# Optimization experiments

Measured on AMD Instinct MI355X. Metric: run time of the kernel, lower is better.

Reference implementation:

```python
import jax, jax.numpy as jnp
import numpy as np

B, C, HH, WW = 4, 128, 64, 64
NH = 2                      # n_heads
D = C // NH                 # head dim
N = HH * WW                 # tokens


def setup_inputs() -> dict:
    key = jax.random.key(0)
    ks = jax.random.split(key, 8)
    s = 1.0 / np.sqrt(C)
    return {
        "x": jax.random.normal(ks[0], (B, C, HH, WW), dtype=jnp.float32),
        "wq": jax.random.normal(ks[1], (C, C), dtype=jnp.float32) * s,
        "bq": jnp.zeros((C,), dtype=jnp.float32),
        "wk": jax.random.normal(ks[2], (C, C), dtype=jnp.float32) * s,
        "bk": jnp.zeros((C,), dtype=jnp.float32),
        "wv": jax.random.normal(ks[3], (C, C), dtype=jnp.float32) * s,
        "bv": jnp.zeros((C,), dtype=jnp.float32),
        "pe": jax.random.normal(ks[4], (N, D, NH), dtype=jnp.float32),
    }


def reference(x, wq, bq, wk, bk, wv, bv, pe):
    b, c, h, w = x.shape
    nh = pe.shape[2]
    d = c // nh
    n = h * w
    xf = x.reshape(b, c, n)                       # flatten spatial -> tokens
    # 1x1 convs == per-pixel channel matmuls
    q = jnp.einsum('oc,bcn->bon', wq, xf) + bq[None, :, None]
    k = jnp.einsum('oc,bcn->bon', wk, xf) + bk[None, :, None]
    v = jnp.einsum('oc,bcn->bon', wv, xf) + bv[None, :, None]
    q = q.reshape(b, nh, d, n)
    k = k.reshape(b, nh, d, n)
    v = v.reshape(b, nh, d, n)
    # learned positional encoding added to q: pe [n, d, nh] -> [nh, d, n]
    q = q + jnp.transpose(pe, (2, 1, 0))[None]
    scale = jnp.asarray(c, x.dtype) ** -0.25
    scores = jnp.einsum('bhdn,bhdm->bhnm', q, k) * scale   # [b,nh,n,n]
    attn = jax.nn.softmax(scores, axis=-1)
    # dropout is identity in eval mode
    o = jnp.einsum('bhnm,bhdm->bhdn', attn, v)             # [b,nh,d,n]
    attn_out = jnp.transpose(o.reshape(b, nh, d, h, w), (0, 2, 1, 3, 4))
    out = attn_out.reshape(b, c, h, w)
    return (out, attn_out)
```

## Files before the change

kernel.cpp:

```cpp
#include <hip/hip_runtime.h>
#include <hip/hip_bf16.h>

typedef unsigned short ushort_t;
typedef unsigned int   uint_t;
typedef unsigned short ushortx8 __attribute__((ext_vector_type(8)));
typedef unsigned short ushortx4 __attribute__((ext_vector_type(4)));
typedef unsigned int   uintx4   __attribute__((ext_vector_type(4)));
typedef __bf16        bf16x8   __attribute__((ext_vector_type(8)));
typedef float         f32x4    __attribute__((ext_vector_type(4)));
typedef float         f32x16   __attribute__((ext_vector_type(16)));

#define SCALE_QL (0.29730177875068026f * 1.4426950408889634f)
#define OUT_HALF 2097152
#define NSPLIT   4
#define KT_SPLIT 16
#define MFIX     32.0f

static __device__ __forceinline__ float fexp2(float x) {
    float r; asm("v_exp_f32 %0, %1" : "=v"(r) : "v"(x)); return r;
}
static __device__ __forceinline__ unsigned cvtpk_bf16(float lo, float hi) {
    unsigned r;
    asm("v_cvt_pk_bf16_f32 %0, %1, %2" : "=v"(r) : "v"(lo), "v"(hi));
    return r;
}
static __device__ __forceinline__ void pswap(unsigned& a, unsigned& b) {
    asm("v_permlane32_swap_b32 %0, %1" : "+v"(a), "+v"(b));
}
static __device__ __forceinline__ ushort_t bf16u(float f) {
    __hip_bfloat16 h = __float2bfloat16(f);
    return __builtin_bit_cast(ushort_t, h);
}
static __device__ __forceinline__ float bflo(unsigned u) {
    return __builtin_bit_cast(float, u << 16);
}
static __device__ __forceinline__ float bfhi(unsigned u) {
    return __builtin_bit_cast(float, u & 0xffff0000u);
}
static __device__ __forceinline__ void glds16(const void* g, void* l) {
    __builtin_amdgcn_global_load_lds(
        (const __attribute__((address_space(1))) unsigned int*)g,
        (__attribute__((address_space(3))) unsigned int*)l, 16, 0, 0);
}

__global__ __launch_bounds__(256) void prep_kernel(
    const float* __restrict__ pe,
    const float* __restrict__ wq, const float* __restrict__ wk,
    const float* __restrict__ wv,
    float* __restrict__ pet, ushort_t* __restrict__ wb)
{
    const int bid = blockIdx.x, t = threadIdx.x;
    if (bid < 1024) {
        int idx = bid * 256 + t;
        float2 p2 = *(const float2*)(pe + (size_t)idx * 2);
        pet[idx]                     = p2.x;
        pet[(size_t)4096 * 64 + idx] = p2.y;
        return;
    }
    const int b2 = bid - 1024;
    const int p  = b2 >> 3;
    const float* w = (p == 0) ? wq : (p == 1) ? wk : wv;
    const int cid = (b2 & 7) * 256 + t;
    const int o = cid >> 4, chunk = cid & 15;
    float4 f0 = *(const float4*)(w + o * 128 + chunk * 8);
    float4 f1 = *(const float4*)(w + o * 128 + chunk * 8 + 4);
    ushortx8 u;
    u[0] = bf16u(f0.x); u[1] = bf16u(f0.y); u[2] = bf16u(f0.z); u[3] = bf16u(f0.w);
    u[4] = bf16u(f1.x); u[5] = bf16u(f1.y); u[6] = bf16u(f1.z); u[7] = bf16u(f1.w);
    *(ushortx8*)(wb + p * 16384 + o * 128 + ((chunk ^ (o & 15)) << 3)) = u;
}

__global__ __launch_bounds__(256) void xt_kernel(const float* __restrict__ x,
                                                 ushort_t* __restrict__ xtb)
{
    const int nt = blockIdx.x, b = blockIdx.y;
    __shared__ __align__(16) ushort_t xs[128][68];
    const int t = threadIdx.x;
    const int cg = t >> 4, n0 = (t & 15) * 4;
#pragma unroll
    for (int i = 0; i < 8; ++i) {
        int c = i * 16 + cg;
        float4 f = *(const float4*)(x + ((size_t)(b * 128 + c)) * 4096 + nt * 64 + n0);
        ushortx4 u;
        u[0] = bf16u(f.x); u[1] = bf16u(f.y); u[2] = bf16u(f.z); u[3] = bf16u(f.w);
        *(ushortx4*)(&xs[c][n0]) = u;
    }
    __syncthreads();
    const int n = t >> 2;
    ushort_t* dst = xtb + ((size_t)b * 4096 + nt * 64 + n) * 128;
#pragma unroll
    for (int j = 0; j < 4; ++j) {
        int chunk = (t & 3) * 4 + j;
        ushortx8 u;
#pragma unroll
        for (int e = 0; e < 8; ++e) u[e] = xs[chunk * 8 + e][n];
        *(ushortx8*)(dst + ((chunk ^ (n & 15)) << 3)) = u;
    }
}

__global__ __launch_bounds__(256, 2) void proj_kernel(
    const ushort_t* __restrict__ xtb, const ushort_t* __restrict__ wb,
    const float* __restrict__ bq, const float* __restrict__ bk,
    const float* __restrict__ bv, const float* __restrict__ pet,
    ushort_t* __restrict__ qw, ushort_t* __restrict__ kw,
    ushort_t* __restrict__ vw)
{
    const int ntl = blockIdx.x;
    const int b = blockIdx.y, p = blockIdx.z;
    __shared__ __align__(16) ushort_t xt[16384];
    __shared__ __align__(16) ushort_t wt[16384];
    const int t = threadIdx.x, lane = t & 63;
    const int wv_ = __builtin_amdgcn_readfirstlane(t >> 6);
    const int l16 = lane & 15, lhi = lane >> 4;

    const ushort_t* xsrc = xtb + ((size_t)b * 4096 + ntl * 128) * 128;
    const ushort_t* wsrc = wb + p * 16384;
#pragma unroll
    for (int j = 0; j < 8; ++j) {
        int row = wv_ * 32 + j * 4;
        glds16(xsrc + row * 128 + lane * 8, xt + row * 128);
        glds16(wsrc + row * 128 + lane * 8, wt + row * 128);
    }

    const float* bias = (p == 0) ? bq : (p == 1) ? bk : bv;
    f32x4 bias4[2];
    bias4[0] = *(const f32x4*)(bias + wv_ * 32 + lhi * 4);
    bias4[1] = *(const f32x4*)(bias + wv_ * 32 + 16 + lhi * 4);
    f32x4 acc[2][8];
#pragma unroll
    for (int mf = 0; mf < 2; ++mf)
#pragma unroll
        for (int nf = 0; nf < 8; ++nf) acc[mf][nf] = bias4[mf];

    __syncthreads();

    const char* xbp = (const char*)xt;
    const char* wbp = (const char*)wt;
#pragma unroll
    for (int ks = 0; ks < 4; ++ks) {
        bf16x8 af[2];
#pragma unroll
        for (int mf = 0; mf < 2; ++mf) {
            int row = wv_ * 32 + mf * 16 + l16;
            af[mf] = __builtin_bit_cast(bf16x8, *(const ushortx8*)(
                wbp + row * 256 + ((((ks * 4 + lhi) ^ l16) & 15) << 4)));
        }
#pragma unroll
        for (int nf = 0; nf < 8; ++nf) {
            int row = nf * 16 + l16;
            bf16x8 bfr = __builtin_bit_cast(bf16x8, *(const ushortx8*)(
                xbp + row * 256 + ((((ks * 4 + lhi) ^ l16) & 15) << 4)));
            acc[0][nf] = __builtin_amdgcn_mfma_f32_16x16x32_bf16(af[0], bfr, acc[0][nf], 0, 0, 0);
            acc[1][nf] = __builtin_amdgcn_mfma_f32_16x16x32_bf16(af[1], bfr, acc[1][nf], 0, 0, 0);
        }
    }

    const int nbase = ntl * 128;
    if (p == 2) {
#pragma unroll
        for (int mf = 0; mf < 2; ++mf) {
            int o = wv_ * 32 + mf * 16 + lhi * 4;
            int h = o >> 6, d = o & 63;
            ushort_t* vb = vw + (((size_t)(b * 2 + h) * 64 + d)) * 4096 + nbase + l16;
#pragma unroll
            for (int nf = 0; nf < 8; ++nf)
#pragma unroll
                for (int r = 0; r < 4; ++r)
                    vb[(size_t)r * 4096 + nf * 16] = bf16u(acc[mf][nf][r]);
        }
    } else if (p == 0) {
#pragma unroll
        for (int mf = 0; mf < 2; ++mf) {
            int o = wv_ * 32 + mf * 16 + lhi * 4;
            int h = o >> 6, d = o & 63;
#pragma unroll
            for (int nf = 0; nf < 8; ++nf) {
                int n = nbase + nf * 16 + l16;
                f32x4 pe4 = *(const f32x4*)(pet + ((size_t)h * 4096 + n) * 64 + d);
                f32x4 q4 = (acc[mf][nf] + pe4) * SCALE_QL;
                ushortx4 s;
                s[0] = bf16u(q4[0]); s[1] = bf16u(q4[1]);
                s[2] = bf16u(q4[2]); s[3] = bf16u(q4[3]);
                *(ushortx4*)(qw + ((size_t)(b * 2 + h) * 4096 + n) * 64 + d) = s;
            }
        }
    } else {
#pragma unroll
        for (int mf = 0; mf < 2; ++mf) {
            int o = wv_ * 32 + mf * 16 + lhi * 4;
            int h = o >> 6, d = o & 63;
#pragma unroll
            for (int nf = 0; nf < 8; ++nf) {
                int n = nbase + nf * 16 + l16;
                f32x4 k4 = acc[mf][nf];
                ushortx4 s;
                s[0] = bf16u(k4[0]); s[1] = bf16u(k4[1]);
                s[2] = bf16u(k4[2]); s[3] = bf16u(k4[3]);
                *(ushortx4*)(kw + ((size_t)(b * 2 + h) * 4096 + n) * 64 + d) = s;
            }
        }
    }
}

__global__ __launch_bounds__(512, 4) void attn_kernel(
    const ushort_t* __restrict__ qw, const ushort_t* __restrict__ kw,
    const ushort_t* __restrict__ vw, uint_t* __restrict__ opart,
    float* __restrict__ lspart)
{
    const int qt = blockIdx.x, bh = blockIdx.y, sp = blockIdx.z;
    const int t = threadIdx.x, lane = t & 63;
    const int wv = t >> 6;
    const int l31 = lane & 31, hi = lane >> 5;

    __shared__ __align__(16) ushort_t Kt[2 * 64 * 64];
    __shared__ __align__(16) ushort_t Vt[2 * 64 * 64];

    const int qb = qt * 256 + wv * 32;
    bf16x8 qf[4];
#pragma unroll
    for (int ks = 0; ks < 4; ++ks)
        qf[ks] = __builtin_bit_cast(bf16x8, *(const ushortx8*)(
            qw + ((size_t)bh * 4096 + qb + l31) * 64 + ks * 16 + hi * 8));

    const ushort_t* kgb = kw + ((size_t)bh * 4096) * 64;
    const ushort_t* vgb = vw + ((size_t)bh * 64) * 4096;

    const int srow = lane >> 3, c7 = lane & 7;
    const int rb = wv * 8;
    const int swz = (c7 ^ srow) << 3;
    const size_t koff = (size_t)(rb + srow) * 64 + swz;
    const size_t voff = (size_t)(rb + srow) * 4096 + swz;

    const f32x16 z16 = {0,0,0,0,0,0,0,0,0,0,0,0,0,0,0,0};
    f32x16 oa0 = z16, oa1 = z16;
    float ls0 = 0.f;

    const int kt0 = sp * KT_SPLIT;

#define STAGE(buf, ktb)                                                       \
    {                                                                         \
        glds16(kgb + (size_t)(ktb) * 4096 + koff,                             \
               Kt + (buf) * 4096 + (size_t)rb * 64);                          \
        glds16(vgb + (size_t)(ktb) * 64 + voff,                               \
               Vt + (buf) * 4096 + (size_t)rb * 64);                          \
    }

    STAGE(0, kt0)
    __syncthreads();

    const int sw7 = l31 & 7;
    int cur = 0;
    for (int it = 0; it < KT_SPLIT; ++it) {
        const int itn = (it + 1 < KT_SPLIT) ? it + 1 : it;
        STAGE(cur ^ 1, kt0 + itn)

        const char* kc = (const char*)(Kt + cur * 4096);
        const char* vc = (const char*)(Vt + cur * 4096);

#pragma unroll
        for (int c = 0; c < 2; ++c) {
            const int kbase = (c * 32 + l31) * 128;
            bf16x8 kf[4];
#pragma unroll
            for (int ks = 0; ks < 4; ++ks)
                kf[ks] = __builtin_bit_cast(bf16x8, *(const ushortx8*)(
                    kc + kbase + (((ks * 2 + hi) ^ sw7) << 4)));

            f32x16 s0 = z16;
            __builtin_amdgcn_s_setprio(1);
#pragma unroll
            for (int ks = 0; ks < 4; ++ks)
                s0 = __builtin_amdgcn_mfma_f32_32x32x16_bf16(kf[ks], qf[ks], s0, 0, 0, 0);
            __builtin_amdgcn_s_setprio(0);

            float p[16];
#pragma unroll
            for (int r = 0; r < 16; ++r) p[r] = fexp2(s0[r] - MFIX);
            float q0 = (p[0] + p[1]) + (p[2] + p[3]);
            float q1 = (p[4] + p[5]) + (p[6] + p[7]);
            float q2 = (p[8] + p[9]) + (p[10] + p[11]);
            float q3 = (p[12] + p[13]) + (p[14] + p[15]);
            float psum = (q0 + q1) + (q2 + q3);
            psum += __shfl_xor(psum, 32, 64);
            ls0 += psum;
            unsigned c0 = cvtpk_bf16(p[0], p[1]);
            unsigned c1 = cvtpk_bf16(p[2], p[3]);
            unsigned c2 = cvtpk_bf16(p[4], p[5]);
            unsigned c3 = cvtpk_bf16(p[6], p[7]);
            unsigned c4 = cvtpk_bf16(p[8], p[9]);
            unsigned c5 = cvtpk_bf16(p[10], p[11]);
            unsigned c6 = cvtpk_bf16(p[12], p[13]);
            unsigned c7x = cvtpk_bf16(p[14], p[15]);
            pswap(c0, c2); pswap(c1, c3); pswap(c4, c6); pswap(c5, c7x);
            bf16x8 pfa, pfb;
            { uintx4 u; u[0] = c0; u[1] = c1; u[2] = c2; u[3] = c3;
              pfa = __builtin_bit_cast(bf16x8, u); }
            { uintx4 u; u[0] = c4; u[1] = c5; u[2] = c6; u[3] = c7x;
              pfb = __builtin_bit_cast(bf16x8, u); }

            __builtin_amdgcn_s_setprio(1);
            {
                const int vb0 = l31 * 128;
                bf16x8 vf0 = __builtin_bit_cast(bf16x8, *(const ushortx8*)(
                    vc + vb0 + ((((c * 2 + 0) * 2 + hi) ^ sw7) << 4)));
                bf16x8 vf1 = __builtin_bit_cast(bf16x8, *(const ushortx8*)(
                    vc + vb0 + ((((c * 2 + 1) * 2 + hi) ^ sw7) << 4)));
                oa0 = __builtin_amdgcn_mfma_f32_32x32x16_bf16(vf0, pfa, oa0, 0, 0, 0);
                oa0 = __builtin_amdgcn_mfma_f32_32x32x16_bf16(vf1, pfb, oa0, 0, 0, 0);
            }
            {
                const int vb1 = (32 + l31) * 128;
                bf16x8 vf0 = __builtin_bit_cast(bf16x8, *(const ushortx8*)(
                    vc + vb1 + ((((c * 2 + 0) * 2 + hi) ^ sw7) << 4)));
                bf16x8 vf1 = __builtin_bit_cast(bf16x8, *(const ushortx8*)(
                    vc + vb1 + ((((c * 2 + 1) * 2 + hi) ^ sw7) << 4)));
                oa1 = __builtin_amdgcn_mfma_f32_32x32x16_bf16(vf0, pfa, oa1, 0, 0, 0);
                oa1 = __builtin_amdgcn_mfma_f32_32x32x16_bf16(vf1, pfb, oa1, 0, 0, 0);
            }
            __builtin_amdgcn_s_setprio(0);
        }

        __syncthreads();
        cur ^= 1;
    }

    const int pidx = (qt * 8 + bh) * NSPLIT + sp;
#define STORE_OA(OA, DT)                                                      \
    {                                                                         \
        uintx4 u0, u1;                                                        \
        u0[0] = cvtpk_bf16(OA[0], OA[1]);  u0[1] = cvtpk_bf16(OA[2], OA[3]);  \
        u0[2] = cvtpk_bf16(OA[4], OA[5]);  u0[3] = cvtpk_bf16(OA[6], OA[7]);  \
        u1[0] = cvtpk_bf16(OA[8], OA[9]);  u1[1] = cvtpk_bf16(OA[10], OA[11]);\
        u1[2] = cvtpk_bf16(OA[12], OA[13]);u1[3] = cvtpk_bf16(OA[14], OA[15]);\
        uint_t* dst = opart +                                                 \
            (((size_t)pidx * 8 + wv) * 2 + (DT)) * 512 + lane * 8;            \
        *(uintx4*)dst = u0; *(uintx4*)(dst + 4) = u1;                         \
    }
    STORE_OA(oa0, 0) STORE_OA(oa1, 1)

    if (hi == 0)
        lspart[(pidx * 8 + wv) * 32 + l31] = ls0;
}

__global__ __launch_bounds__(512) void combine_kernel(
    const uint_t* __restrict__ opart, const float* __restrict__ lspart,
    float* __restrict__ out)
{
    const int qt = blockIdx.x, bh = blockIdx.y;
    const int b = bh >> 1, h = bh & 1;
    const int t = threadIdx.x, lane = t & 63, wa = t >> 6;
    const int l31 = lane & 31, hi = lane >> 5;
    const int pbase = (qt * 8 + bh) * NSPLIT;
    const int dtbl[8] = {0, 2, 8, 10, 16, 18, 24, 26};

    float den = 0.f;
#pragma unroll
    for (int sp = 0; sp < NSPLIT; ++sp)
        den += lspart[((pbase + sp) * 8 + wa) * 32 + l31];
    float inv = 1.f / den;

    const int q = qt * 256 + wa * 32 + l31;
#pragma unroll
    for (int dt = 0; dt < 2; ++dt) {
        float acc[16];
#pragma unroll
        for (int i = 0; i < 16; ++i) acc[i] = 0.f;
#pragma unroll
        for (int sp = 0; sp < NSPLIT; ++sp) {
            const uint_t* src = opart +
                (((size_t)(pbase + sp) * 8 + wa) * 2 + dt) * 512 + lane * 8;
            uintx4 a = *(const uintx4*)src;
            uintx4 b2 = *(const uintx4*)(src + 4);
#pragma unroll
            for (int j = 0; j < 4; ++j) {
                acc[2 * j]     += bflo(a[j]);
                acc[2 * j + 1] += bfhi(a[j]);
                acc[8 + 2 * j] += bflo(b2[j]);
                acc[9 + 2 * j] += bfhi(b2[j]);
            }
        }
#pragma unroll
        for (int j = 0; j < 8; ++j) {
            int d = dt * 32 + 4 * hi + dtbl[j];
            float v0 = acc[2 * j] * inv;
            float v1 = acc[2 * j + 1] * inv;
            size_t o0 = ((size_t)(b * 128 + d * 2 + h)) * 4096 + q;
            out[o0] = v0;
            out[o0 + OUT_HALF] = v0;
            size_t o1 = o0 + 2 * 4096;
            out[o1] = v1;
            out[o1 + OUT_HALF] = v1;
        }
    }
}

extern "C" void kernel_launch(void* const* d_in, const int* in_sizes, int n_in,
                              void* d_out, int out_size, void* d_ws, size_t ws_size,
                              hipStream_t stream) {
    const float* x  = (const float*)d_in[0];
    const float* wq = (const float*)d_in[1];
    const float* bq = (const float*)d_in[2];
    const float* wk = (const float*)d_in[3];
    const float* bk = (const float*)d_in[4];
    const float* wv = (const float*)d_in[5];
    const float* bv = (const float*)d_in[6];
    const float* pe = (const float*)d_in[7];
    float* out = (float*)d_out;

    char* ws = (char*)d_ws;
    float*    pet   = (float*)ws;
    ushort_t* qw    = (ushort_t*)(ws + (size_t)2  * 1024 * 1024);
    ushort_t* kw    = (ushort_t*)(ws + (size_t)6  * 1024 * 1024);
    ushort_t* vw    = (ushort_t*)(ws + (size_t)10 * 1024 * 1024);
    uint_t*   opart = (uint_t*)(ws + (size_t)14 * 1024 * 1024);
    ushort_t* xtb   = (ushort_t*)(ws + (size_t)14 * 1024 * 1024);
    float*    lsprt = (float*)(ws + (size_t)31 * 1024 * 1024);
    ushort_t* wb    = (ushort_t*)(ws + (size_t)31 * 1024 * 1024);

    hipLaunchKernelGGL(prep_kernel, dim3(1048), dim3(256), 0, stream,
                       pe, wq, wk, wv, pet, wb);
    hipLaunchKernelGGL(xt_kernel, dim3(64, 4), dim3(256), 0, stream, x, xtb);
    hipLaunchKernelGGL(proj_kernel, dim3(32, 4, 3), dim3(256), 0, stream,
                       xtb, wb, bq, bk, bv, pet, qw, kw, vw);
    hipLaunchKernelGGL(attn_kernel, dim3(16, 8, NSPLIT), dim3(512), 0, stream,
                       qw, kw, vw, opart, lsprt);
    hipLaunchKernelGGL(combine_kernel, dim3(16, 8), dim3(512), 0, stream,
                       opart, lsprt, out);
}
```

Baseline: 76.10 us.

## Fuse x transpose into projection kernel and loop over Q/K/V per block

Drops the separate xt_kernel. The projection kernel now loads fp32 x directly, converts it to bf16 and transposes it in shared memory, then loops over the three weight matrices (Q, K, V) reusing the same x tile. This removes one kernel launch and the global round trip through the xtb buffer, at the cost of a smaller token tile per block (64 instead of 128) and serialized weight loads inside each block. Separately, the attention kernel's cross-half row-sum shuffle is moved out of the inner loop to a single shuffle at the end.

```diff
diff --git a/kernel.cpp b/kernel.cpp
--- a/kernel.cpp
+++ b/kernel.cpp
@@ -70,133 +70,134 @@
     *(ushortx8*)(wb + p * 16384 + o * 128 + ((chunk ^ (o & 15)) << 3)) = u;
 }
 
-__global__ __launch_bounds__(256) void xt_kernel(const float* __restrict__ x,
-                                                 ushort_t* __restrict__ xtb)
-{
-    const int nt = blockIdx.x, b = blockIdx.y;
-    __shared__ __align__(16) ushort_t xs[128][68];
-    const int t = threadIdx.x;
-    const int cg = t >> 4, n0 = (t & 15) * 4;
-#pragma unroll
-    for (int i = 0; i < 8; ++i) {
-        int c = i * 16 + cg;
-        float4 f = *(const float4*)(x + ((size_t)(b * 128 + c)) * 4096 + nt * 64 + n0);
-        ushortx4 u;
-        u[0] = bf16u(f.x); u[1] = bf16u(f.y); u[2] = bf16u(f.z); u[3] = bf16u(f.w);
-        *(ushortx4*)(&xs[c][n0]) = u;
-    }
-    __syncthreads();
-    const int n = t >> 2;
-    ushort_t* dst = xtb + ((size_t)b * 4096 + nt * 64 + n) * 128;
-#pragma unroll
-    for (int j = 0; j < 4; ++j) {
-        int chunk = (t & 3) * 4 + j;
-        ushortx8 u;
-#pragma unroll
-        for (int e = 0; e < 8; ++e) u[e] = xs[chunk * 8 + e][n];
-        *(ushortx8*)(dst + ((chunk ^ (n & 15)) << 3)) = u;
-    }
-}
-
 __global__ __launch_bounds__(256, 2) void proj_kernel(
-    const ushort_t* __restrict__ xtb, const ushort_t* __restrict__ wb,
+    const float* __restrict__ x, const ushort_t* __restrict__ wb,
     const float* __restrict__ bq, const float* __restrict__ bk,
     const float* __restrict__ bv, const float* __restrict__ pet,
     ushort_t* __restrict__ qw, ushort_t* __restrict__ kw,
     ushort_t* __restrict__ vw)
 {
     const int ntl = blockIdx.x;
-    const int b = blockIdx.y, p = blockIdx.z;
-    __shared__ __align__(16) ushort_t xt[16384];
-    __shared__ __align__(16) ushort_t wt[16384];
+    const int b = blockIdx.y;
+    __shared__ __align__(16) ushort_t xt[64 * 128];
+    __shared__ __align__(16) union {
+        ushort_t xs[128][68];
+        ushort_t wt[16384];
+    } smu;
     const int t = threadIdx.x, lane = t & 63;
     const int wv_ = __builtin_amdgcn_readfirstlane(t >> 6);
     const int l16 = lane & 15, lhi = lane >> 4;
 
-    const ushort_t* xsrc = xtb + ((size_t)b * 4096 + ntl * 128) * 128;
-    const ushort_t* wsrc = wb + p * 16384;
-#pragma unroll
-    for (int j = 0; j < 8; ++j) {
-        int row = wv_ * 32 + j * 4;
-        glds16(xsrc + row * 128 + lane * 8, xt + row * 128);
-        glds16(wsrc + row * 128 + lane * 8, wt + row * 128);
-    }
-
-    const float* bias = (p == 0) ? bq : (p == 1) ? bk : bv;
-    f32x4 bias4[2];
-    bias4[0] = *(const f32x4*)(bias + wv_ * 32 + lhi * 4);
-    bias4[1] = *(const f32x4*)(bias + wv_ * 32 + 16 + lhi * 4);
-    f32x4 acc[2][8];
-#pragma unroll
-    for (int mf = 0; mf < 2; ++mf)
-#pragma unroll
-        for (int nf = 0; nf < 8; ++nf) acc[mf][nf] = bias4[mf];
-
+    {
+        const int cg = t >> 4, n0 = (t & 15) * 4;
+#pragma unroll
+        for (int i = 0; i < 8; ++i) {
+            int c = i * 16 + cg;
+            float4 f = *(const float4*)(x + ((size_t)(b * 128 + c)) * 4096 + ntl * 64 + n0);
+            ushortx4 u;
+            u[0] = bf16u(f.x); u[1] = bf16u(f.y); u[2] = bf16u(f.z); u[3] = bf16u(f.w);
+            *(ushortx4*)(&smu.xs[c][n0]) = u;
+        }
+    }
     __syncthreads();
-
+    {
+        const int n = t >> 2;
+#pragma unroll
+        for (int j = 0; j < 4; ++j) {
+            int chunk = (t & 3) * 4 + j;
+            ushortx8 u;
+#pragma unroll
+            for (int e = 0; e < 8; ++e) u[e] = smu.xs[chunk * 8 + e][n];
+            *(ushortx8*)(xt + n * 128 + ((chunk ^ (n & 15)) << 3)) = u;
+        }
+    }
+
+    const int nbase = ntl * 64;
     const char* xbp = (const char*)xt;
-    const char* wbp = (const char*)wt;
-#pragma unroll
-    for (int ks = 0; ks < 4; ++ks) {
-        bf16x8 af[2];
-#pragma unroll
-        for (int mf = 0; mf < 2; ++mf) {
-            int row = wv_ * 32 + mf * 16 + l16;
-            af[mf] = __builtin_bit_cast(bf16x8, *(const ushortx8*)(
-                wbp + row * 256 + ((((ks * 4 + lhi) ^ l16) & 15) << 4)));
-        }
-#pragma unroll
-        for (int nf = 0; nf < 8; ++nf) {
-            int row = nf * 16 + l16;
-            bf16x8 bfr = __builtin_bit_cast(bf16x8, *(const ushortx8*)(
-                xbp + row * 256 + ((((ks * 4 + lhi) ^ l16) & 15) << 4)));
-            acc[0][nf] = __builtin_amdgcn_mfma_f32_16x16x32_bf16(af[0], bfr, acc[0][nf], 0, 0, 0);
-            acc[1][nf] = __builtin_amdgcn_mfma_f32_16x16x32_bf16(af[1], bfr, acc[1][nf], 0, 0, 0);
-        }
-    }
-
-    const int nbase = ntl * 128;
-    if (p == 2) {
-#pragma unroll
-        for (int mf = 0; mf < 2; ++mf) {
-            int o = wv_ * 32 + mf * 16 + lhi * 4;
-            int h = o >> 6, d = o & 63;
-            ushort_t* vb = vw + (((size_t)(b * 2 + h) * 64 + d)) * 4096 + nbase + l16;
-#pragma unroll
-            for (int nf = 0; nf < 8; ++nf)
-#pragma unroll
-                for (int r = 0; r < 4; ++r)
-                    vb[(size_t)r * 4096 + nf * 16] = bf16u(acc[mf][nf][r]);
-        }
-    } else if (p == 0) {
-#pragma unroll
-        for (int mf = 0; mf < 2; ++mf) {
-            int o = wv_ * 32 + mf * 16 + lhi * 4;
-            int h = o >> 6, d = o & 63;
-#pragma unroll
-            for (int nf = 0; nf < 8; ++nf) {
-                int n = nbase + nf * 16 + l16;
-                f32x4 pe4 = *(const f32x4*)(pet + ((size_t)h * 4096 + n) * 64 + d);
-                f32x4 q4 = (acc[mf][nf] + pe4) * SCALE_QL;
-                ushortx4 s;
-                s[0] = bf16u(q4[0]); s[1] = bf16u(q4[1]);
-                s[2] = bf16u(q4[2]); s[3] = bf16u(q4[3]);
-                *(ushortx4*)(qw + ((size_t)(b * 2 + h) * 4096 + n) * 64 + d) = s;
-            }
-        }
-    } else {
-#pragma unroll
-        for (int mf = 0; mf < 2; ++mf) {
-            int o = wv_ * 32 + mf * 16 + lhi * 4;
-            int h = o >> 6, d = o & 63;
-#pragma unroll
-            for (int nf = 0; nf < 8; ++nf) {
-                int n = nbase + nf * 16 + l16;
-                f32x4 k4 = acc[mf][nf];
-                ushortx4 s;
-                s[0] = bf16u(k4[0]); s[1] = bf16u(k4[1]);
-                s[2] = bf16u(k4[2]); s[3] = bf16u(k4[3]);
-                *(ushortx4*)(kw + ((size_t)(b * 2 + h) * 4096 + n) * 64 + d) = s;
+    const char* wbp = (const char*)smu.wt;
+
+    for (int p = 0; p < 3; ++p) {
+        __syncthreads();
+        const ushort_t* wsrc = wb + p * 16384;
+#pragma unroll
+        for (int j = 0; j < 8; ++j) {
+            int row = wv_ * 32 + j * 4;
+            glds16(wsrc + row * 128 + lane * 8, smu.wt + row * 128);
+        }
+
+        const float* bias = (p == 0) ? bq : (p == 1) ? bk : bv;
+        f32x4 bias4[2];
+        bias4[0] = *(const f32x4*)(bias + wv_ * 32 + lhi * 4);
+        bias4[1] = *(const f32x4*)(bias + wv_ * 32 + 16 + lhi * 4);
+        f32x4 acc[2][4];
+#pragma unroll
+        for (int mf = 0; mf < 2; ++mf)
+#pragma unroll
+            for (int nf = 0; nf < 4; ++nf) acc[mf][nf] = bias4[mf];
+
+        __syncthreads();
+
+#pragma unroll
+        for (int ks = 0; ks < 4; ++ks) {
+            bf16x8 af[2];
+#pragma unroll
+            for (int mf = 0; mf < 2; ++mf) {
+                int row = wv_ * 32 + mf * 16 + l16;
+                af[mf] = __builtin_bit_cast(bf16x8, *(const ushortx8*)(
+                    wbp + row * 256 + ((((ks * 4 + lhi) ^ l16) & 15) << 4)));
+            }
+#pragma unroll
+            for (int nf = 0; nf < 4; ++nf) {
+                int row = nf * 16 + l16;
+                bf16x8 bfr = __builtin_bit_cast(bf16x8, *(const ushortx8*)(
+                    xbp + row * 256 + ((((ks * 4 + lhi) ^ l16) & 15) << 4)));
+                acc[0][nf] = __builtin_amdgcn_mfma_f32_16x16x32_bf16(af[0], bfr, acc[0][nf], 0, 0, 0);
+                acc[1][nf] = __builtin_amdgcn_mfma_f32_16x16x32_bf16(af[1], bfr, acc[1][nf], 0, 0, 0);
+            }
+        }
+
+        if (p == 2) {
+#pragma unroll
+            for (int mf = 0; mf < 2; ++mf) {
+                int o = wv_ * 32 + mf * 16 + lhi * 4;
+                int h = o >> 6, d = o & 63;
+                ushort_t* vb = vw + (((size_t)(b * 2 + h) * 64 + d)) * 4096 + nbase + l16;
+#pragma unroll
+                for (int nf = 0; nf < 4; ++nf)
+#pragma unroll
+                    for (int r = 0; r < 4; ++r)
+                        vb[(size_t)r * 4096 + nf * 16] = bf16u(acc[mf][nf][r]);
+            }
+        } else if (p == 0) {
+#pragma unroll
+            for (int mf = 0; mf < 2; ++mf) {
+                int o = wv_ * 32 + mf * 16 + lhi * 4;
+                int h = o >> 6, d = o & 63;
+#pragma unroll
+                for (int nf = 0; nf < 4; ++nf) {
+                    int n = nbase + nf * 16 + l16;
+                    f32x4 pe4 = *(const f32x4*)(pet + ((size_t)h * 4096 + n) * 64 + d);
+                    f32x4 q4 = (acc[mf][nf] + pe4) * SCALE_QL;
+                    ushortx4 s;
+                    s[0] = bf16u(q4[0]); s[1] = bf16u(q4[1]);
+                    s[2] = bf16u(q4[2]); s[3] = bf16u(q4[3]);
+                    *(ushortx4*)(qw + ((size_t)(b * 2 + h) * 4096 + n) * 64 + d) = s;
+                }
+            }
+        } else {
+#pragma unroll
+            for (int mf = 0; mf < 2; ++mf) {
+                int o = wv_ * 32 + mf * 16 + lhi * 4;
+                int h = o >> 6, d = o & 63;
+#pragma unroll
+                for (int nf = 0; nf < 4; ++nf) {
+                    int n = nbase + nf * 16 + l16;
+                    f32x4 k4 = acc[mf][nf];
+                    ushortx4 s;
+                    s[0] = bf16u(k4[0]); s[1] = bf16u(k4[1]);
+                    s[2] = bf16u(k4[2]); s[3] = bf16u(k4[3]);
+                    *(ushortx4*)(kw + ((size_t)(b * 2 + h) * 4096 + n) * 64 + d) = s;
+                }
             }
         }
     }
@@ -280,9 +281,7 @@
             float q1 = (p[4] + p[5]) + (p[6] + p[7]);
             float q2 = (p[8] + p[9]) + (p[10] + p[11]);
             float q3 = (p[12] + p[13]) + (p[14] + p[15]);
-            float psum = (q0 + q1) + (q2 + q3);
-            psum += __shfl_xor(psum, 32, 64);
-            ls0 += psum;
+            ls0 += (q0 + q1) + (q2 + q3);
             unsigned c0 = cvtpk_bf16(p[0], p[1]);
             unsigned c1 = cvtpk_bf16(p[2], p[3]);
             unsigned c2 = cvtpk_bf16(p[4], p[5]);
@@ -338,6 +337,7 @@
     }
     STORE_OA(oa0, 0) STORE_OA(oa1, 1)
 
+    ls0 += __shfl_xor(ls0, 32, 64);
     if (hi == 0)
         lspart[(pidx * 8 + wv) * 32 + l31] = ls0;
 }
@@ -413,15 +413,13 @@
     ushort_t* kw    = (ushort_t*)(ws + (size_t)6  * 1024 * 1024);
     ushort_t* vw    = (ushort_t*)(ws + (size_t)10 * 1024 * 1024);
     uint_t*   opart = (uint_t*)(ws + (size_t)14 * 1024 * 1024);
-    ushort_t* xtb   = (ushort_t*)(ws + (size_t)14 * 1024 * 1024);
     float*    lsprt = (float*)(ws + (size_t)31 * 1024 * 1024);
     ushort_t* wb    = (ushort_t*)(ws + (size_t)31 * 1024 * 1024);
 
     hipLaunchKernelGGL(prep_kernel, dim3(1048), dim3(256), 0, stream,
                        pe, wq, wk, wv, pet, wb);
-    hipLaunchKernelGGL(xt_kernel, dim3(64, 4), dim3(256), 0, stream, x, xtb);
-    hipLaunchKernelGGL(proj_kernel, dim3(32, 4, 3), dim3(256), 0, stream,
-                       xtb, wb, bq, bk, bv, pet, qw, kw, vw);
+    hipLaunchKernelGGL(proj_kernel, dim3(64, 4), dim3(256), 0, stream,
+                       x, wb, bq, bk, bv, pet, qw, kw, vw);
     hipLaunchKernelGGL(attn_kernel, dim3(16, 8, NSPLIT), dim3(512), 0, stream,
                        qw, kw, vw, opart, lsprt);
     hipLaunchKernelGGL(combine_kernel, dim3(16, 8), dim3(512), 0, stream,
```

New measurement: 70.53 us. 1.08x faster.
